# Optimization experiments

Measured on AMD Instinct MI355X. Metric: run time of the kernel, lower is better.

The kernel has to match this reference:

```python
import jax, jax.numpy as jnp
import numpy as np

N_WIRES = 10
DEPTH = 2
BATCH = 16384
DIM = 2 ** N_WIRES
N_ENC = min(N_WIRES, 4)


def _cnot_perm(n, c, t):
    # wire 0 is the most-significant bit (torchquantum convention)
    idx = np.arange(2 ** n)
    ctrl = (idx >> (n - 1 - c)) & 1
    return idx ^ (ctrl << (n - 1 - t))


def _ring_perm(n):
    # composition of CNOT(0,1)...CNOT(n-2,n-1), CNOT(n-1,0) as one basis permutation
    perm = np.arange(2 ** n)
    for w in range(n - 1):
        perm = perm[_cnot_perm(n, w, w + 1)]
    perm = perm[_cnot_perm(n, n - 1, 0)]
    return perm


RING_PERM = jnp.asarray(_ring_perm(N_WIRES))
_idx = np.arange(DIM)
# Z_SIGNS[i, w] = +1 if bit of wire w in basis state i is 0, else -1
Z_SIGNS = jnp.asarray(np.stack(
    [1.0 - 2.0 * ((_idx >> (N_WIRES - 1 - w)) & 1) for w in range(N_WIRES)],
    axis=1).astype(np.float32))  # (DIM, N_WIRES)


def _apply_rx(st, cos_h, sin_h, w):
    # RX(theta) = [[cos(t/2), -i sin(t/2)], [-i sin(t/2), cos(t/2)]] on wire w
    # st: (B, DIM) complex64; cos_h/sin_h: scalar (shared param) or (B,) (encoder)
    b = st.shape[0]
    st = st.reshape(b, 2 ** w, 2, -1)
    a0 = st[:, :, 0, :]
    a1 = st[:, :, 1, :]
    c = jnp.reshape(cos_h, (-1, 1, 1))
    s = jnp.reshape(sin_h, (-1, 1, 1))
    n0 = c * a0 - 1j * s * a1
    n1 = -1j * s * a0 + c * a1
    return jnp.stack([n0, n1], axis=2).reshape(b, -1)


def setup_inputs() -> dict:
    key = jax.random.key(0)
    k1, k2 = jax.random.split(key)
    x = jax.random.normal(k1, (BATCH, N_ENC), dtype=jnp.float32)
    theta = 0.1 * jax.random.normal(k2, (N_WIRES,), dtype=jnp.float32)
    return {"x": x, "theta": theta}


def reference(x, theta):
    b = x.shape[0]
    # |0...0> initial state
    st = jnp.zeros((b, DIM), dtype=jnp.complex64).at[:, 0].set(1.0)
    # encoder: RX(x[:, i]) on wire i
    half = x * 0.5
    for i in range(N_ENC):
        st = _apply_rx(st, jnp.cos(half[:, i]), jnp.sin(half[:, i]), i)
    ct = jnp.cos(theta * 0.5)
    sn = jnp.sin(theta * 0.5)
    for _ in range(DEPTH):
        for w in range(N_WIRES):
            st = _apply_rx(st, ct[w], sn[w], w)
        st = st[:, RING_PERM]  # fused CNOT ring
    probs = jnp.real(st * jnp.conj(st))  # (B, DIM)
    return probs @ Z_SIGNS  # (B, N_WIRES) PauliZ expectations
```

## Files before the change

### kernel.cpp

```cpp
#include <hip/hip_runtime.h>
#include <math.h>

#define BATCH 16384
#define NW 10
#define NENC 4
#define DEPTH 2


__global__ __launch_bounds__(256) void k1_basis(const float* __restrict__ theta,
                                                float2* __restrict__ u)
{
    const int lane = threadIdx.x & 63;
    const int a = (blockIdx.x * blockDim.x + threadIdx.x) >> 6;

    float re[16], im[16];
#pragma unroll
    for (int r = 0; r < 16; ++r) { re[r] = 0.0f; im[r] = 0.0f; }
    if (lane == 0) re[a] = 1.0f;

    float ct[NW], st_[NW];
#pragma unroll
    for (int w = 0; w < NW; ++w) {
        const float h = 0.5f * theta[w];
        ct[w] = __cosf(h); st_[w] = __sinf(h);
    }

#pragma unroll 1
    for (int d = 0; d < DEPTH; ++d) {
#pragma unroll
        for (int w = 0; w < 4; ++w) {
            const float c = ct[w], s = st_[w];
            const int m = 8 >> w;
#pragma unroll
            for (int r = 0; r < 16; ++r) {
                if (!(r & m)) {
                    const int r1 = r | m;
                    const float a0r = re[r],  a0i = im[r];
                    const float a1r = re[r1], a1i = im[r1];
                    re[r]  = c * a0r + s * a1i;
                    im[r]  = c * a0i - s * a1r;
                    re[r1] = c * a1r + s * a0i;
                    im[r1] = c * a1i - s * a0r;
                }
            }
        }
#pragma unroll
        for (int w = 4; w < 10; ++w) {
            const float c = ct[w], s = st_[w];
            const int lm = 32 >> (w - 4);
#pragma unroll
            for (int r = 0; r < 16; ++r) {
                const float pr = __shfl_xor(re[r], lm, 64);
                const float pi = __shfl_xor(im[r], lm, 64);
                re[r] = c * re[r] + s * pi;
                im[r] = c * im[r] - s * pr;
            }
        }
#pragma unroll
        for (int w = 0; w < 3; ++w) {
            const int cm = 8 >> w, tm = 8 >> (w + 1);
#pragma unroll
            for (int r = 0; r < 16; ++r) {
                if ((r & cm) && !(r & tm)) {
                    const int r2 = r | tm;
                    float t;
                    t = re[r]; re[r] = re[r2]; re[r2] = t;
                    t = im[r]; im[r] = im[r2]; im[r2] = t;
                }
            }
        }
#pragma unroll
        for (int r = 0; r < 16; ++r) {
            if (r & 1) {
                re[r] = __shfl_xor(re[r], 32, 64);
                im[r] = __shfl_xor(im[r], 32, 64);
            }
        }
#pragma unroll
        for (int w = 4; w < 9; ++w) {
            const int cm = 32 >> (w - 4), tm = 32 >> (w - 3);
            const bool ctl = (lane & cm) != 0;
#pragma unroll
            for (int r = 0; r < 16; ++r) {
                const float pr = __shfl_xor(re[r], tm, 64);
                const float pi = __shfl_xor(im[r], tm, 64);
                re[r] = ctl ? pr : re[r];
                im[r] = ctl ? pi : im[r];
            }
        }
        {
            const bool ctl = (lane & 1) != 0;
#pragma unroll
            for (int r = 0; r < 8; ++r) {
                const float t0r = re[r], t1r = re[r + 8];
                const float t0i = im[r], t1i = im[r + 8];
                re[r]     = ctl ? t1r : t0r;
                re[r + 8] = ctl ? t0r : t1r;
                im[r]     = ctl ? t1i : t0i;
                im[r + 8] = ctl ? t0i : t1i;
            }
        }
    }

#pragma unroll
    for (int r = 0; r < 16; ++r)
        u[a * 1024 + (r << 6) + lane] = make_float2(re[r], im[r]);
}

__global__ __launch_bounds__(256) void k2_gram(const float2* __restrict__ u,
                                               float* __restrict__ C)
{
    const int lane = threadIdx.x & 63;
    const int q = (blockIdx.x * blockDim.x + threadIdx.x) >> 6;
    const int a = q >> 4, b = q & 15;

    float Sr[NW], Si[NW];
#pragma unroll
    for (int w = 0; w < NW; ++w) { Sr[w] = 0.0f; Si[w] = 0.0f; }

#pragma unroll
    for (int t = 0; t < 16; ++t) {
        const int i = t * 64 + lane;
        const float2 ua = u[a * 1024 + i];
        const float2 ub = u[b * 1024 + i];
        const float vr = ua.x * ub.x + ua.y * ub.y;
        const float vi = ua.x * ub.y - ua.y * ub.x;
#pragma unroll
        for (int w = 0; w < NW; ++w) {
            const int mask = 1 << (9 - w);
            const float sv = (i & mask) ? -1.0f : 1.0f;
            Sr[w] = fmaf(sv, vr, Sr[w]);
            Si[w] = fmaf(sv, vi, Si[w]);
        }
    }
#pragma unroll
    for (int w = 0; w < NW; ++w) {
        float r = Sr[w], ii = Si[w];
#pragma unroll
        for (int ofs = 32; ofs >= 1; ofs >>= 1) {
            r  += __shfl_xor(r,  ofs, 64);
            ii += __shfl_xor(ii, ofs, 64);
        }
        Sr[w] = r; Si[w] = ii;
    }

    if (lane == 0) {
        const int p = (__popc(a) - __popc(b)) & 3;
#pragma unroll
        for (int w = 0; w < NW; ++w) {
            const float sr = Sr[w], si = Si[w];
            const float c = (p == 0) ? sr : (p == 1) ? -si : (p == 2) ? -sr : si;
            C[q * 12 + w] = c;
        }
    }
}

__global__ __launch_bounds__(832) void k2b_xform(const float* __restrict__ C,
                                                 float* __restrict__ K)
{
    const int tid = threadIdx.x;
    if (tid >= 810) return;
    const int t = tid / 10, w = tid - 10 * t;
    int d0 = t / 27, r0 = t - d0 * 27;
    int d1 = r0 / 9, r1 = r0 - d1 * 9;
    int d2 = r1 / 3, d3 = r1 - d2 * 3;
    const int d[4] = { d0, d1, d2, d3 };

    float s = 0.0f;
#pragma unroll
    for (int e = 0; e < 16; ++e) {
        int a = 0, b = 0; float sg = 1.0f;
#pragma unroll
        for (int q = 0; q < 4; ++q) {
            const int eq = (e >> (3 - q)) & 1;
            int aq, bq;
            if (d[q] == 2) { aq = eq; bq = 1 - eq; }
            else {
                aq = eq; bq = eq;
                if (d[q] == 1 && eq) sg = -sg;
            }
            a |= aq << (3 - q);
            b |= bq << (3 - q);
        }
        s += sg * C[(a * 16 + b) * 12 + w];
    }
    K[t * 12 + w] = s * 0.0625f;
}

__global__ __launch_bounds__(128) void k3_eval(const float* __restrict__ x,
                                               const float* __restrict__ K,
                                               float* __restrict__ out)
{
    __shared__ float lK[81 * 12];
    for (int i = threadIdx.x; i < 81 * 12; i += 128) lK[i] = K[i];
    __syncthreads();

    const int bidx = blockIdx.x * 128 + threadIdx.x;
    const float4 xv = ((const float4*)x)[bidx];

    float s0, c0, s1, c1, s2, c2, s3, c3;
    __sincosf(xv.x, &s0, &c0);
    __sincosf(xv.y, &s1, &c1);
    __sincosf(xv.z, &s2, &c2);
    __sincosf(xv.w, &s3, &c3);

    const float b0[3] = { 1.0f, c0, s0 };
    const float b1[3] = { 1.0f, c1, s1 };
    const float b2[3] = { 1.0f, c2, s2 };
    const float b3[3] = { 1.0f, c3, s3 };
    float B01[9], B23[9];
#pragma unroll
    for (int i = 0; i < 3; ++i)
#pragma unroll
        for (int j = 0; j < 3; ++j) {
            B01[i * 3 + j] = b0[i] * b1[j];
            B23[i * 3 + j] = b2[i] * b3[j];
        }

    float z[NW];
#pragma unroll
    for (int w = 0; w < NW; ++w) z[w] = 0.0f;

#pragma unroll
    for (int t01 = 0; t01 < 9; ++t01) {
#pragma unroll
        for (int t23 = 0; t23 < 9; ++t23) {
            const float P = B01[t01] * B23[t23];
            const float* base = &lK[(t01 * 9 + t23) * 12];
            const float4 q0 = *(const float4*)(base + 0);
            const float4 q1 = *(const float4*)(base + 4);
            const float4 q2 = *(const float4*)(base + 8);
            z[0] = fmaf(P, q0.x, z[0]);
            z[1] = fmaf(P, q0.y, z[1]);
            z[2] = fmaf(P, q0.z, z[2]);
            z[3] = fmaf(P, q0.w, z[3]);
            z[4] = fmaf(P, q1.x, z[4]);
            z[5] = fmaf(P, q1.y, z[5]);
            z[6] = fmaf(P, q1.z, z[6]);
            z[7] = fmaf(P, q1.w, z[7]);
            z[8] = fmaf(P, q2.x, z[8]);
            z[9] = fmaf(P, q2.y, z[9]);
        }
    }

    float2* po = (float2*)(out + bidx * NW);
    po[0] = make_float2(z[0], z[1]);
    po[1] = make_float2(z[2], z[3]);
    po[2] = make_float2(z[4], z[5]);
    po[3] = make_float2(z[6], z[7]);
    po[4] = make_float2(z[8], z[9]);
}

extern "C" void kernel_launch(void* const* d_in, const int* in_sizes, int n_in,
                              void* d_out, int out_size, void* d_ws, size_t ws_size,
                              hipStream_t stream) {
    const float* x     = (const float*)d_in[0];
    const float* theta = (const float*)d_in[1];
    float* out = (float*)d_out;

    float2* u = (float2*)d_ws;
    float*  C = (float*)((char*)d_ws + 16 * 1024 * sizeof(float2));
    float*  K = C + 256 * 12;

    hipLaunchKernelGGL(k1_basis,  dim3(4),   dim3(256), 0, stream, theta, u);
    hipLaunchKernelGGL(k2_gram,   dim3(64),  dim3(256), 0, stream, u, C);
    hipLaunchKernelGGL(k2b_xform, dim3(1),   dim3(832), 0, stream, C, K);
    hipLaunchKernelGGL(k3_eval,   dim3(BATCH / 128), dim3(128), 0, stream, x, K, out);
}
```

Measured before the change: 80.34 us.

## Fuse all four kernels into one cooperative kernel with grid sync

Replaces the basis, Gram, transform and eval kernels with a single cooperative kernel of 128 blocks. Each wave recomputes its two basis columns in registers, so the unitary is never written to or read from global memory, and the sign-weighted reduction is restructured to use register-index and lane-bit signs. After a grid-wide sync, every block redundantly computes the 81x10 K table in shared memory and then evaluates its 128 batch rows. This removes three kernel launches and their dependencies. In exchange it adds grid-sync cost, duplicates the column simulation 16-fold across waves, and duplicates the K transform in every block.

```diff
diff --git a/kernel.cpp b/kernel.cpp
--- a/kernel.cpp
+++ b/kernel.cpp
@@ -1,29 +1,21 @@
 #include <hip/hip_runtime.h>
+#include <hip/hip_cooperative_groups.h>
 #include <math.h>
 
 #define BATCH 16384
 #define NW 10
-#define NENC 4
 #define DEPTH 2
 
-
-__global__ __launch_bounds__(256) void k1_basis(const float* __restrict__ theta,
-                                                float2* __restrict__ u)
+namespace cg = cooperative_groups;
+
+
+__device__ __forceinline__ void sim_column(int a, int lane,
+                                           const float* ct, const float* st_,
+                                           float re[16], float im[16])
 {
-    const int lane = threadIdx.x & 63;
-    const int a = (blockIdx.x * blockDim.x + threadIdx.x) >> 6;
-
-    float re[16], im[16];
 #pragma unroll
     for (int r = 0; r < 16; ++r) { re[r] = 0.0f; im[r] = 0.0f; }
     if (lane == 0) re[a] = 1.0f;
-
-    float ct[NW], st_[NW];
-#pragma unroll
-    for (int w = 0; w < NW; ++w) {
-        const float h = 0.5f * theta[w];
-        ct[w] = __cosf(h); st_[w] = __sinf(h);
-    }
 
 #pragma unroll 1
     for (int d = 0; d < DEPTH; ++d) {
@@ -101,98 +93,107 @@
             }
         }
     }
-
-#pragma unroll
-    for (int r = 0; r < 16; ++r)
-        u[a * 1024 + (r << 6) + lane] = make_float2(re[r], im[r]);
 }
 
-__global__ __launch_bounds__(256) void k2_gram(const float2* __restrict__ u,
-                                               float* __restrict__ C)
+__global__ __launch_bounds__(128) void fused_all(const float* __restrict__ x,
+                                                 const float* __restrict__ theta,
+                                                 float* __restrict__ out,
+                                                 float* __restrict__ Cg)
 {
     const int lane = threadIdx.x & 63;
-    const int q = (blockIdx.x * blockDim.x + threadIdx.x) >> 6;
-    const int a = q >> 4, b = q & 15;
-
-    float Sr[NW], Si[NW];
-#pragma unroll
-    for (int w = 0; w < NW; ++w) { Sr[w] = 0.0f; Si[w] = 0.0f; }
-
-#pragma unroll
-    for (int t = 0; t < 16; ++t) {
-        const int i = t * 64 + lane;
-        const float2 ua = u[a * 1024 + i];
-        const float2 ub = u[b * 1024 + i];
-        const float vr = ua.x * ub.x + ua.y * ub.y;
-        const float vi = ua.x * ub.y - ua.y * ub.x;
+    const int wv   = threadIdx.x >> 6;
+    const int q    = blockIdx.x * 2 + wv;
+    const int a    = q >> 4, b = q & 15;
+
+    {
+        float ct[NW], st_[NW];
 #pragma unroll
         for (int w = 0; w < NW; ++w) {
-            const int mask = 1 << (9 - w);
-            const float sv = (i & mask) ? -1.0f : 1.0f;
-            Sr[w] = fmaf(sv, vr, Sr[w]);
-            Si[w] = fmaf(sv, vi, Si[w]);
-        }
-    }
-#pragma unroll
-    for (int w = 0; w < NW; ++w) {
-        float r = Sr[w], ii = Si[w];
-#pragma unroll
-        for (int ofs = 32; ofs >= 1; ofs >>= 1) {
-            r  += __shfl_xor(r,  ofs, 64);
-            ii += __shfl_xor(ii, ofs, 64);
-        }
-        Sr[w] = r; Si[w] = ii;
-    }
-
-    if (lane == 0) {
+            const float h = 0.5f * theta[w];
+            ct[w] = __cosf(h); st_[w] = __sinf(h);
+        }
+
+        float ar[16], ai[16], br[16], bi[16];
+        sim_column(a, lane, ct, st_, ar, ai);
+        sim_column(b, lane, ct, st_, br, bi);
+
         const int p = (__popc(a) - __popc(b)) & 3;
-#pragma unroll
-        for (int w = 0; w < NW; ++w) {
-            const float sr = Sr[w], si = Si[w];
-            const float c = (p == 0) ? sr : (p == 1) ? -si : (p == 2) ? -sr : si;
-            C[q * 12 + w] = c;
-        }
-    }
-}
-
-__global__ __launch_bounds__(832) void k2b_xform(const float* __restrict__ C,
-                                                 float* __restrict__ K)
-{
-    const int tid = threadIdx.x;
-    if (tid >= 810) return;
-    const int t = tid / 10, w = tid - 10 * t;
-    int d0 = t / 27, r0 = t - d0 * 27;
-    int d1 = r0 / 9, r1 = r0 - d1 * 9;
-    int d2 = r1 / 3, d3 = r1 - d2 * 3;
-    const int d[4] = { d0, d1, d2, d3 };
-
-    float s = 0.0f;
-#pragma unroll
-    for (int e = 0; e < 16; ++e) {
-        int a = 0, b = 0; float sg = 1.0f;
-#pragma unroll
-        for (int q = 0; q < 4; ++q) {
-            const int eq = (e >> (3 - q)) & 1;
-            int aq, bq;
-            if (d[q] == 2) { aq = eq; bq = 1 - eq; }
-            else {
-                aq = eq; bq = eq;
-                if (d[q] == 1 && eq) sg = -sg;
-            }
-            a |= aq << (3 - q);
-            b |= bq << (3 - q);
-        }
-        s += sg * C[(a * 16 + b) * 12 + w];
-    }
-    K[t * 12 + w] = s * 0.0625f;
-}
-
-__global__ __launch_bounds__(128) void k3_eval(const float* __restrict__ x,
-                                               const float* __restrict__ K,
-                                               float* __restrict__ out)
-{
-    __shared__ float lK[81 * 12];
-    for (int i = threadIdx.x; i < 81 * 12; i += 128) lK[i] = K[i];
+        const bool odd = (p & 1) != 0;
+
+        float red[10];
+#pragma unroll
+        for (int k = 0; k < 10; ++k) red[k] = 0.0f;
+#pragma unroll
+        for (int r = 0; r < 16; ++r) {
+            const float vr = ar[r] * br[r] + ai[r] * bi[r];
+            const float vi = ar[r] * bi[r] - ai[r] * br[r];
+            const float v  = odd ? vi : vr;
+            red[0] += (r & 8) ? -v : v;
+            red[1] += (r & 4) ? -v : v;
+            red[2] += (r & 2) ? -v : v;
+            red[3] += (r & 1) ? -v : v;
+            red[4] += v;
+        }
+        const float T = red[4];
+        red[4] = (lane & 32) ? -T : T;
+        red[5] = (lane & 16) ? -T : T;
+        red[6] = (lane &  8) ? -T : T;
+        red[7] = (lane &  4) ? -T : T;
+        red[8] = (lane &  2) ? -T : T;
+        red[9] = (lane &  1) ? -T : T;
+
+#pragma unroll
+        for (int k = 0; k < 10; ++k) {
+            float v = red[k];
+#pragma unroll
+            for (int ofs = 32; ofs >= 1; ofs >>= 1)
+                v += __shfl_xor(v, ofs, 64);
+            red[k] = v;
+        }
+
+        if (lane == 0) {
+            const float sg = (p == 1 || p == 2) ? -1.0f : 1.0f;
+#pragma unroll
+            for (int w = 0; w < NW; ++w)
+                Cg[q * 12 + w] = sg * red[w];
+        }
+    }
+
+    __threadfence();
+    cg::this_grid().sync();
+
+    __shared__ float sC[256 * 12];
+    __shared__ float sK[81 * 12];
+    for (int i = threadIdx.x; i < 256 * 12; i += 128) sC[i] = Cg[i];
+    __syncthreads();
+
+    for (int idx = threadIdx.x; idx < 810; idx += 128) {
+        const int t = idx / 10, w = idx - 10 * t;
+        int d0 = t / 27, r0 = t - d0 * 27;
+        int d1 = r0 / 9, r1 = r0 - d1 * 9;
+        int d2 = r1 / 3, d3 = r1 - d2 * 3;
+        const int d[4] = { d0, d1, d2, d3 };
+
+        float s = 0.0f;
+#pragma unroll
+        for (int e = 0; e < 16; ++e) {
+            int aa = 0, bb = 0; float sgn = 1.0f;
+#pragma unroll
+            for (int qq = 0; qq < 4; ++qq) {
+                const int eq = (e >> (3 - qq)) & 1;
+                int aq, bq;
+                if (d[qq] == 2) { aq = eq; bq = 1 - eq; }
+                else {
+                    aq = eq; bq = eq;
+                    if (d[qq] == 1 && eq) sgn = -sgn;
+                }
+                aa |= aq << (3 - qq);
+                bb |= bq << (3 - qq);
+            }
+            s += sgn * sC[(aa * 16 + bb) * 12 + w];
+        }
+        sK[t * 12 + w] = s * 0.0625f;
+    }
     __syncthreads();
 
     const int bidx = blockIdx.x * 128 + threadIdx.x;
@@ -226,7 +227,7 @@
 #pragma unroll
         for (int t23 = 0; t23 < 9; ++t23) {
             const float P = B01[t01] * B23[t23];
-            const float* base = &lK[(t01 * 9 + t23) * 12];
+            const float* base = &sK[(t01 * 9 + t23) * 12];
             const float4 q0 = *(const float4*)(base + 0);
             const float4 q1 = *(const float4*)(base + 4);
             const float4 q2 = *(const float4*)(base + 8);
@@ -257,13 +258,9 @@
     const float* x     = (const float*)d_in[0];
     const float* theta = (const float*)d_in[1];
     float* out = (float*)d_out;
-
-    float2* u = (float2*)d_ws;
-    float*  C = (float*)((char*)d_ws + 16 * 1024 * sizeof(float2));
-    float*  K = C + 256 * 12;
-
-    hipLaunchKernelGGL(k1_basis,  dim3(4),   dim3(256), 0, stream, theta, u);
-    hipLaunchKernelGGL(k2_gram,   dim3(64),  dim3(256), 0, stream, u, C);
-    hipLaunchKernelGGL(k2b_xform, dim3(1),   dim3(832), 0, stream, C, K);
-    hipLaunchKernelGGL(k3_eval,   dim3(BATCH / 128), dim3(128), 0, stream, x, K, out);
+    float* Cg  = (float*)d_ws;
+
+    void* args[] = { (void*)&x, (void*)&theta, (void*)&out, (void*)&Cg };
+    hipLaunchCooperativeKernel((void*)fused_all, dim3(128), dim3(128),
+                               args, 0, stream);
 }
```

Measured after the change: 110.9 us. +38.1%, slower.
